# Kernel tuning notes

Hardware: AMD Instinct MI355X
Metric: run time of the kernel (lower is better)

Reference implementation:

```python
import jax, jax.numpy as jnp
import numpy as np

ROOT_2 = 1.41421
C = 256
DIV = 4
CP = C // DIV  # 64


def _spectral_normalize(w2d):
    # exact largest singular value (torch uses power iteration approx of this)
    s = jnp.linalg.norm(w2d, ord=2)
    return w2d / s


def setup_inputs() -> dict:
    key = jax.random.key(0)
    ks = jax.random.split(key, 10)
    B, H, W = 8, 64, 64
    x = jax.random.normal(ks[0], (B, C, H, W), dtype=jnp.float32)
    # 1x1 conv weights stored as [out, in]; spectral-normalized like torch's spectral_norm
    def conv_w(k, o, i):
        w = jax.random.normal(k, (o, i), dtype=jnp.float32) * (1.0 / np.sqrt(i))
        return _spectral_normalize(w)
    Wq = conv_w(ks[1], CP, C); bq = jnp.zeros((CP,), jnp.float32)
    Wk = conv_w(ks[2], CP, C); bk = jnp.zeros((CP,), jnp.float32)
    Wv = conv_w(ks[3], CP, C); bv = jnp.zeros((CP,), jnp.float32)
    Wo = conv_w(ks[4], C, CP); bo = jnp.zeros((C,), jnp.float32)
    gamma = jnp.zeros((1,), jnp.float32)
    return {"x": x, "Wq": Wq, "bq": bq, "Wk": Wk, "bk": bk,
            "Wv": Wv, "bv": bv, "Wo": Wo, "bo": bo, "gamma": gamma}


def reference(x, Wq, bq, Wk, bk, Wv, bv, Wo, bo, gamma):
    B, c, h, w = x.shape
    n = h * w
    const1 = jnp.float32(ROOT_2 / np.sqrt(C))       # Weight_Scaling(in_channels)
    const2 = jnp.float32(ROOT_2 / np.sqrt(CP))      # Weight_Scaling(in_channels//div_num)
    xs = (const1 * x).reshape(B, c, n)              # [B,C,N]
    q = jnp.einsum('oc,bcn->bon', Wq, xs) + bq[None, :, None]  # [B,C',N]
    k = jnp.einsum('oc,bcn->bon', Wk, xs) + bk[None, :, None]
    v = jnp.einsum('oc,bcn->bon', Wv, xs) + bv[None, :, None]
    # attn[b,i,j] = softmax_j(q[:,i]^T k[:,j])
    scores = jnp.einsum('bcn,bcm->bnm', q, k)       # [B,N,N]
    attn = jax.nn.softmax(scores, axis=-1)
    sa = jnp.einsum('bcm,bnm->bcn', v, attn)        # v @ attn^T
    sa = const2 * sa
    out = jnp.einsum('oc,bcn->bon', Wo, sa) + bo[None, :, None]  # [B,C,N]
    out = out.reshape(B, c, h, w)
    return gamma[0] * out + x
```

## Files before the change

kernel.cpp:

```cpp
#include <hip/hip_runtime.h>


#define Bsz 8
#define Cch 256
#define CPd 64
#define Nn  4096
#define TIL 64
#define QROWS 128
#define NSPL 4
#define MQUAR (Nn / NSPL)

typedef __attribute__((ext_vector_type(8))) short short8;
typedef __attribute__((ext_vector_type(4))) float f32x4;

static constexpr float C1 = (float)(1.41421 / 16.0);
static constexpr float C2 = (float)(1.41421 / 8.0);

__device__ inline unsigned pk_trunc(float lo, float hi) {
    return __builtin_amdgcn_perm(__float_as_uint(hi), __float_as_uint(lo), 0x07060302u);
}
__device__ inline float dpp_swap1(float v) {
    return __uint_as_float((unsigned)__builtin_amdgcn_mov_dpp(
        (int)__float_as_uint(v), 0xB1, 0xF, 0xF, true));
}
__device__ __forceinline__ void gl16(const unsigned short* g, unsigned short* s) {
    __builtin_amdgcn_global_load_lds(
        (const __attribute__((address_space(1))) void*)g,
        (__attribute__((address_space(3))) void*)s, 16, 0, 0);
}

__global__ __launch_bounds__(256) void wconv_kernel(
    const float* __restrict__ Wq, const float* __restrict__ Wk,
    const float* __restrict__ Wv, const float* __restrict__ Wo,
    unsigned short* __restrict__ Wb)
{
    const int idx = (blockIdx.x * 256 + threadIdx.x) * 4;
    const float* src = (idx < 16384) ? Wq : (idx < 32768) ? Wk : (idx < 49152) ? Wv : Wo;
    const float4 v = *(const float4*)(src + (idx & 16383));
    *(uint2*)(Wb + idx) = make_uint2(pk_trunc(v.x, v.y), pk_trunc(v.z, v.w));
}

__global__ __launch_bounds__(256) void qkv_kernel(
    const float* __restrict__ x, const unsigned short* __restrict__ Wb,
    const float* __restrict__ bq, const float* __restrict__ bk, const float* __restrict__ bv,
    unsigned short* __restrict__ qT, unsigned short* __restrict__ kT,
    unsigned short* __restrict__ vB)
{
    __shared__ __align__(16) unsigned short Wlds[CPd * 264];
    __shared__ __align__(16) float T[TIL * 68];

    const int b   = blockIdx.y;
    const int n0  = blockIdx.x * TIL;
    const int t   = threadIdx.x;
    const int g   = t >> 6;
    const int l15 = t & 15;
    const int l4  = (t & 63) >> 4;

    const float* xb = x + (size_t)b * Cch * Nn + n0 + 16 * g + l15;
    short8 xf[8];
    #pragma unroll
    for (int ks = 0; ks < 8; ++ks) {
        float xr[8];
        #pragma unroll
        for (int j = 0; j < 8; ++j)
            xr[j] = C1 * xb[(size_t)(8 * l4 + 32 * ks + j) * Nn];
        union { unsigned u[4]; short8 s; } p;
        p.u[0] = pk_trunc(xr[0], xr[1]); p.u[1] = pk_trunc(xr[2], xr[3]);
        p.u[2] = pk_trunc(xr[4], xr[5]); p.u[3] = pk_trunc(xr[6], xr[7]);
        xf[ks] = p.s;
    }

    #pragma unroll
    for (int mat = 0; mat < 3; ++mat) {
        {
            const uint4* wg = (const uint4*)(Wb + mat * 16384);
            #pragma unroll
            for (int p = 0; p < 8; ++p) {
                const int idx = p * 256 + t;
                const int o = idx >> 5, cs = idx & 31;
                *(uint4*)&Wlds[o * 264 + cs * 8] = wg[idx];
            }
        }
        __syncthreads();

        const float* bias = (mat == 0) ? bq : (mat == 1) ? bk : bv;
        f32x4 acc[4];
        #pragma unroll
        for (int st = 0; st < 4; ++st) {
            const float bb = bias[16 * st + l15];
            acc[st] = (f32x4){bb, bb, bb, bb};
        }
        #pragma unroll
        for (int st = 0; st < 4; ++st) {
            #pragma unroll
            for (int ks = 0; ks < 8; ++ks) {
                const short8 wf = *(const short8*)&Wlds[(16 * st + l15) * 264 + 8 * l4 + 32 * ks];
                acc[st] = __builtin_amdgcn_mfma_f32_16x16x32_bf16(xf[ks], wf, acc[st], 0, 0, 0);
            }
        }
        __syncthreads();

        if (mat < 2) {
            #pragma unroll
            for (int st = 0; st < 4; ++st)
                #pragma unroll
                for (int r = 0; r < 4; ++r)
                    T[(16 * g + 4 * l4 + r) * 68 + 16 * st + l15] = acc[st][r];
        } else {
            #pragma unroll
            for (int st = 0; st < 4; ++st)
                #pragma unroll
                for (int r = 0; r < 4; ++r)
                    T[(16 * st + l15) * 68 + 16 * g + 4 * l4 + r] = acc[st][r];
        }
        __syncthreads();

        const int row = t >> 2;
        const int sg  = 16 * (t & 3);
        const float4 a0 = *(const float4*)&T[row * 68 + sg + 0];
        const float4 a1 = *(const float4*)&T[row * 68 + sg + 4];
        const float4 a2 = *(const float4*)&T[row * 68 + sg + 8];
        const float4 a3 = *(const float4*)&T[row * 68 + sg + 12];
        const uint4 lo = make_uint4(pk_trunc(a0.x, a0.y), pk_trunc(a0.z, a0.w),
                                    pk_trunc(a1.x, a1.y), pk_trunc(a1.z, a1.w));
        const uint4 hi = make_uint4(pk_trunc(a2.x, a2.y), pk_trunc(a2.z, a2.w),
                                    pk_trunc(a3.x, a3.y), pk_trunc(a3.z, a3.w));
        unsigned short* dst;
        if (mat < 2) {
            dst = (mat == 0 ? qT : kT) + ((size_t)(b * Nn + n0 + row)) * CPd + sg;
        } else {
            dst = vB + ((size_t)(b * CPd + row)) * Nn + n0 + sg;
        }
        *(uint4*)dst = lo;
        *(uint4*)(dst + 8) = hi;
    }
}

__global__ __launch_bounds__(512, 6) void flash_kernel(
    const unsigned short* __restrict__ qT, const unsigned short* __restrict__ kT,
    const unsigned short* __restrict__ vB, float* __restrict__ Op, float* __restrict__ Lg)
{
    __shared__ __align__(16) unsigned short Ks0[TIL * 64];
    __shared__ __align__(16) unsigned short Ks1[TIL * 64];
    __shared__ __align__(16) unsigned short Vs0[TIL * 64];
    __shared__ __align__(16) unsigned short Vs1[TIL * 64];
    __shared__ __align__(16) unsigned Pb[QROWS * 34];

    const int b   = blockIdx.y;
    const int n0  = blockIdx.x * QROWS;
    const int s   = blockIdx.z;
    const int t   = threadIdx.x;
    const int l   = t & 63;
    const int w   = t >> 6;
    const int l15 = l & 15;
    const int l4  = l >> 4;
    const int par = l & 1;
    const unsigned sel = par ? 0x03020706u : 0x07060302u;
    const int l15h = l15 >> 1;

    const unsigned short* qp = qT + (size_t)(b * Nn + n0 + 16 * w + l15) * CPd + 8 * l4;
    const short8 qf0 = *(const short8*)qp;
    const short8 qf1 = *(const short8*)(qp + 32);

    f32x4 acco[4];
    #pragma unroll
    for (int ct = 0; ct < 4; ++ct) acco[ct] = (f32x4){0.f, 0.f, 0.f, 0.f};
    float Lp[4] = {0.f, 0.f, 0.f, 0.f};

    const int r8  = l >> 3;
    const int sch = (l & 7) ^ r8;
    const unsigned short* kPtr = kT + (size_t)b * Nn * CPd
                               + (size_t)(8 * w + r8) * CPd + 8 * sch;
    const unsigned short* vPtr = vB + (size_t)b * CPd * Nn
                               + (size_t)(8 * w + r8) * Nn + 8 * sch;
    const int ldsOff = 8 * w * 64;

    const int h7  = l15 & 7;
    const int sw0 = (l4 ^ h7) << 4;

    const int mbase = s * MQUAR;
    const int nt = MQUAR / TIL;

    auto STAGE = [&](unsigned short* KD, unsigned short* VD, int m0) {
        gl16(kPtr + (size_t)m0 * CPd, KD + ldsOff);
        gl16(vPtr + m0,               VD + ldsOff);
    };
    auto COMPUTE = [&](const unsigned short* Kb, const unsigned short* Vb) {
        const char* KsB = (const char*)Kb + (l15 << 7);
        const char* VsB = (const char*)Vb + (l15 << 7);
        f32x4 accs[4];
        __builtin_amdgcn_s_setprio(1);
        #pragma unroll
        for (int st = 0; st < 4; ++st) {
            accs[st] = (f32x4){0.f, 0.f, 0.f, 0.f};
            const short8 kf0 = *(const short8*)(KsB + (st << 11) + sw0);
            const short8 kf1 = *(const short8*)(KsB + (st << 11) + (sw0 ^ 64));
            accs[st] = __builtin_amdgcn_mfma_f32_16x16x32_bf16(qf0, kf0, accs[st], 0, 0, 0);
            accs[st] = __builtin_amdgcn_mfma_f32_16x16x32_bf16(qf1, kf1, accs[st], 0, 0, 0);
        }
        __builtin_amdgcn_s_setprio(0);
        #pragma unroll
        for (int st = 0; st < 4; ++st) {
            unsigned u[4];
            #pragma unroll
            for (int r = 0; r < 4; ++r) {
                float p = __expf(accs[st][r]);
                Lp[r] += p;
                float nb = dpp_swap1(p);
                u[r] = __builtin_amdgcn_perm(__float_as_uint(nb), __float_as_uint(p), sel);
            }
            const int rb = 16 * w + 4 * l4 + 2 * par;
            Pb[(rb + 0) * 34 + 8 * st + l15h] = u[2 * par];
            Pb[(rb + 1) * 34 + 8 * st + l15h] = u[2 * par + 1];
        }
        __builtin_amdgcn_s_setprio(1);
        #pragma unroll
        for (int ks = 0; ks < 2; ++ks) {
            const short8 pf = *(const short8*)&Pb[(16 * w + l15) * 34 + 4 * l4 + 16 * ks];
            const int swk = sw0 ^ (ks << 6);
            #pragma unroll
            for (int ct = 0; ct < 4; ++ct) {
                const short8 vf = *(const short8*)(VsB + (ct << 11) + swk);
                acco[ct] = __builtin_amdgcn_mfma_f32_16x16x32_bf16(pf, vf, acco[ct], 0, 0, 0);
            }
        }
        __builtin_amdgcn_s_setprio(0);
    };

    STAGE(Ks0, Vs0, mbase);
    __syncthreads();
    for (int ti = 0; ti < nt; ti += 2) {
        const int m0 = mbase + ti * TIL;
        STAGE(Ks1, Vs1, m0 + TIL);
        COMPUTE(Ks0, Vs0);
        __syncthreads();
        if (ti + 2 < nt) STAGE(Ks0, Vs0, m0 + 2 * TIL);
        COMPUTE(Ks1, Vs1);
        __syncthreads();
    }

    #pragma unroll
    for (int r = 0; r < 4; ++r) {
        float v = Lp[r];
        v += __shfl_xor(v, 1, 64); v += __shfl_xor(v, 2, 64);
        v += __shfl_xor(v, 4, 64); v += __shfl_xor(v, 8, 64);
        Lp[r] = v;
    }
    if (l15 == 0) {
        #pragma unroll
        for (int r = 0; r < 4; ++r)
            atomicAdd(&Lg[(size_t)b * Nn + n0 + 16 * w + 4 * l4 + r], Lp[r]);
    }
    float* ob = Op + ((size_t)(b * Nn + n0 + 16 * w)) * CPd;
    #pragma unroll
    for (int r = 0; r < 4; ++r) {
        const int nl = 4 * l4 + r;
        #pragma unroll
        for (int ct = 0; ct < 4; ++ct)
            atomicAdd(&ob[(size_t)nl * CPd + 16 * ct + l15], acco[ct][r]);
    }
}

__global__ __launch_bounds__(512) void out_kernel(
    const float* __restrict__ Op, const float* __restrict__ Lg,
    const unsigned short* __restrict__ Wob,
    const float* __restrict__ bo, const float* __restrict__ gamma,
    const float* __restrict__ x, float* __restrict__ y)
{
    __shared__ __align__(16) unsigned short Wos[Cch * 72];
    __shared__ __align__(16) unsigned short Sas[TIL * 72];
    __shared__ float bos[Cch];

    const int b   = blockIdx.y;
    const int n0  = blockIdx.x * TIL;
    const int t   = threadIdx.x;
    const int l   = t & 63;
    const int w   = t >> 6;
    const int l15 = l & 15;
    const int l4  = l >> 4;

    if (t < Cch) bos[t] = bo[t];
    {
        const uint4* wg = (const uint4*)Wob;
        #pragma unroll
        for (int p = 0; p < 4; ++p) {
            const int idx = p * 512 + t;
            const int row = idx >> 3, seg = idx & 7;
            *(uint4*)&Wos[row * 72 + seg * 8] = wg[idx];
        }
    }
    if (t < 256) {
        const int n = t >> 2, seg = t & 3;
        const float* o0 = Op + ((size_t)(b * Nn + n0 + n)) * CPd + seg * 16;
        const float sc = C2 / Lg[(size_t)b * Nn + n0 + n];
        unsigned pk[8];
        #pragma unroll
        for (int i = 0; i < 4; ++i) {
            const float4 a = ((const float4*)o0)[i];
            pk[2 * i]     = pk_trunc(a.x * sc, a.y * sc);
            pk[2 * i + 1] = pk_trunc(a.z * sc, a.w * sc);
        }
        *(uint4*)&Sas[n * 72 + seg * 16]     = make_uint4(pk[0], pk[1], pk[2], pk[3]);
        *(uint4*)&Sas[n * 72 + seg * 16 + 8] = make_uint4(pk[4], pk[5], pk[6], pk[7]);
    }
    __syncthreads();

    short8 bfr[4][2];
    #pragma unroll
    for (int ns = 0; ns < 4; ++ns) {
        bfr[ns][0] = *(const short8*)&Sas[(16 * ns + l15) * 72 + 8 * l4];
        bfr[ns][1] = *(const short8*)&Sas[(16 * ns + l15) * 72 + 8 * l4 + 32];
    }
    const float gam = gamma[0];
    const float* xb = x + (size_t)b * Cch * Nn;
    float*       yb = y + (size_t)b * Cch * Nn;

    #pragma unroll
    for (int os2 = 0; os2 < 2; ++os2) {
        const int obase = 16 * (w + 8 * os2);
        const short8 af0 = *(const short8*)&Wos[(obase + l15) * 72 + 8 * l4];
        const short8 af1 = *(const short8*)&Wos[(obase + l15) * 72 + 8 * l4 + 32];
        #pragma unroll
        for (int ns = 0; ns < 4; ++ns) {
            f32x4 acc = (f32x4){0.f, 0.f, 0.f, 0.f};
            acc = __builtin_amdgcn_mfma_f32_16x16x32_bf16(af0, bfr[ns][0], acc, 0, 0, 0);
            acc = __builtin_amdgcn_mfma_f32_16x16x32_bf16(af1, bfr[ns][1], acc, 0, 0, 0);
            #pragma unroll
            for (int r = 0; r < 4; ++r) {
                const int o = obase + 4 * l4 + r;
                const size_t idx = (size_t)o * Nn + n0 + 16 * ns + l15;
                yb[idx] = fmaf(gam, acc[r] + bos[o], xb[idx]);
            }
        }
    }
}

extern "C" void kernel_launch(void* const* d_in, const int* in_sizes, int n_in,
                              void* d_out, int out_size, void* d_ws, size_t ws_size,
                              hipStream_t stream)
{
    (void)in_sizes; (void)n_in; (void)out_size; (void)ws_size;
    const float* x     = (const float*)d_in[0];
    const float* Wq    = (const float*)d_in[1];
    const float* bq    = (const float*)d_in[2];
    const float* Wk    = (const float*)d_in[3];
    const float* bk    = (const float*)d_in[4];
    const float* Wv    = (const float*)d_in[5];
    const float* bv    = (const float*)d_in[6];
    const float* Wo    = (const float*)d_in[7];
    const float* bo    = (const float*)d_in[8];
    const float* gamma = (const float*)d_in[9];
    float* y = (float*)d_out;

    const size_t per = (size_t)Bsz * Nn * CPd;
    unsigned short* qT = (unsigned short*)d_ws;
    unsigned short* kT = qT + per;
    unsigned short* vB = kT + per;
    float* Op = (float*)(vB + per);
    float* Lg = Op + per;
    unsigned short* Wb = (unsigned short*)(Lg + (size_t)Bsz * Nn);

    hipMemsetAsync(Op, 0, (per + (size_t)Bsz * Nn) * sizeof(float), stream);

    dim3 grid(Nn / TIL, Bsz);
    dim3 gridF(Nn / QROWS, Bsz, NSPL);
    wconv_kernel<<<64, 256, 0, stream>>>(Wq, Wk, Wv, Wo, Wb);
    qkv_kernel<<<grid, 256, 0, stream>>>(x, Wb, bq, bk, bv, qT, kT, vB);
    flash_kernel<<<gridF, 512, 0, stream>>>(qT, kT, vB, Op, Lg);
    out_kernel<<<grid, 512, 0, stream>>>(Op, Lg, Wb + 3 * 16384, bo, gamma, x, y);
}
```

Measured before the change: 178.7 us.

## Single-buffer K with mid-tile barrier, XOR-swizzle P tile, fold memset into QKV kernel

The flash kernel now keeps one K buffer and double-buffers only V. The next K tile is staged after a barrier placed between the QK MFMAs and the softmax. This frees LDS so the occupancy hint can rise from 6 to 8 blocks. The padded P buffer is replaced by an XOR-swizzled 32-word row layout to avoid bank conflicts without padding. The separate hipMemsetAsync for the partial accumulators is folded into the qkv kernel as a grid-stride zero loop, which removes a launch but adds stores to that kernel and adds an extra barrier per tile.

```diff
diff --git a/kernel.cpp b/kernel.cpp
--- a/kernel.cpp
+++ b/kernel.cpp
@@ -44,7 +44,7 @@
     const float* __restrict__ x, const unsigned short* __restrict__ Wb,
     const float* __restrict__ bq, const float* __restrict__ bk, const float* __restrict__ bv,
     unsigned short* __restrict__ qT, unsigned short* __restrict__ kT,
-    unsigned short* __restrict__ vB)
+    unsigned short* __restrict__ vB, float* __restrict__ Opz)
 {
     __shared__ __align__(16) unsigned short Wlds[CPd * 264];
     __shared__ __align__(16) float T[TIL * 68];
@@ -55,6 +55,13 @@
     const int g   = t >> 6;
     const int l15 = t & 15;
     const int l4  = (t & 63) >> 4;
+
+    {
+        const int tid = (blockIdx.y * gridDim.x + blockIdx.x) * 256 + t;
+        float4* z = (float4*)Opz;
+        for (int i = tid; i < 532480; i += 131072)
+            z[i] = make_float4(0.f, 0.f, 0.f, 0.f);
+    }
 
     const float* xb = x + (size_t)b * Cch * Nn + n0 + 16 * g + l15;
     short8 xf[8];
@@ -136,15 +143,14 @@
     }
 }
 
-__global__ __launch_bounds__(512, 6) void flash_kernel(
+__global__ __launch_bounds__(512, 8) void flash_kernel(
     const unsigned short* __restrict__ qT, const unsigned short* __restrict__ kT,
     const unsigned short* __restrict__ vB, float* __restrict__ Op, float* __restrict__ Lg)
 {
-    __shared__ __align__(16) unsigned short Ks0[TIL * 64];
-    __shared__ __align__(16) unsigned short Ks1[TIL * 64];
+    __shared__ __align__(16) unsigned short Ks[TIL * 64];
     __shared__ __align__(16) unsigned short Vs0[TIL * 64];
     __shared__ __align__(16) unsigned short Vs1[TIL * 64];
-    __shared__ __align__(16) unsigned Pb[QROWS * 34];
+    __shared__ __align__(16) unsigned Pb[QROWS * 32];
 
     const int b   = blockIdx.y;
     const int n0  = blockIdx.x * QROWS;
@@ -177,17 +183,22 @@
 
     const int h7  = l15 & 7;
     const int sw0 = (l4 ^ h7) << 4;
+    const char* KsB = (const char*)Ks + (l15 << 7);
 
     const int mbase = s * MQUAR;
     const int nt = MQUAR / TIL;
 
-    auto STAGE = [&](unsigned short* KD, unsigned short* VD, int m0) {
-        gl16(kPtr + (size_t)m0 * CPd, KD + ldsOff);
-        gl16(vPtr + m0,               VD + ldsOff);
-    };
-    auto COMPUTE = [&](const unsigned short* Kb, const unsigned short* Vb) {
-        const char* KsB = (const char*)Kb + (l15 << 7);
-        const char* VsB = (const char*)Vb + (l15 << 7);
+    auto STAGE_K = [&](int m0) { gl16(kPtr + (size_t)m0 * CPd, Ks + ldsOff); };
+    auto STAGE_V = [&](unsigned short* VD, int m0) { gl16(vPtr + m0, VD + ldsOff); };
+
+    STAGE_K(mbase);
+    STAGE_V(Vs0, mbase);
+    __syncthreads();
+
+    for (int ti = 0; ti < nt; ++ti) {
+        const int m1 = mbase + (ti + 1) * TIL;
+        if (ti + 1 < nt) STAGE_V(((ti + 1) & 1) ? Vs1 : Vs0, m1);
+
         f32x4 accs[4];
         __builtin_amdgcn_s_setprio(1);
         #pragma unroll
@@ -199,6 +210,11 @@
             accs[st] = __builtin_amdgcn_mfma_f32_16x16x32_bf16(qf1, kf1, accs[st], 0, 0, 0);
         }
         __builtin_amdgcn_s_setprio(0);
+
+        asm volatile("s_waitcnt lgkmcnt(0)" ::: "memory");
+        __builtin_amdgcn_s_barrier();
+        if (ti + 1 < nt) STAGE_K(m1);
+
         #pragma unroll
         for (int st = 0; st < 4; ++st) {
             unsigned u[4];
@@ -209,14 +225,19 @@
                 float nb = dpp_swap1(p);
                 u[r] = __builtin_amdgcn_perm(__float_as_uint(nb), __float_as_uint(p), sel);
             }
-            const int rb = 16 * w + 4 * l4 + 2 * par;
-            Pb[(rb + 0) * 34 + 8 * st + l15h] = u[2 * par];
-            Pb[(rb + 1) * 34 + 8 * st + l15h] = u[2 * par + 1];
-        }
+            const int rb  = 16 * w + 4 * l4 + 2 * par;
+            const int ch  = 2 * st + (l15h >> 2);
+            const int wic = l15h & 3;
+            Pb[(rb + 0) * 32 + ((ch ^ ((rb)     & 7)) << 2) + wic] = u[2 * par];
+            Pb[(rb + 1) * 32 + ((ch ^ ((rb + 1) & 7)) << 2) + wic] = u[2 * par + 1];
+        }
+
+        const char* VsB = (const char*)((ti & 1) ? Vs1 : Vs0) + (l15 << 7);
         __builtin_amdgcn_s_setprio(1);
         #pragma unroll
         for (int ks = 0; ks < 2; ++ks) {
-            const short8 pf = *(const short8*)&Pb[(16 * w + l15) * 34 + 4 * l4 + 16 * ks];
+            const int pswz = ((l4 + 4 * ks) ^ h7) << 2;
+            const short8 pf = *(const short8*)&Pb[(16 * w + l15) * 32 + pswz];
             const int swk = sw0 ^ (ks << 6);
             #pragma unroll
             for (int ct = 0; ct < 4; ++ct) {
@@ -225,17 +246,7 @@
             }
         }
         __builtin_amdgcn_s_setprio(0);
-    };
-
-    STAGE(Ks0, Vs0, mbase);
-    __syncthreads();
-    for (int ti = 0; ti < nt; ti += 2) {
-        const int m0 = mbase + ti * TIL;
-        STAGE(Ks1, Vs1, m0 + TIL);
-        COMPUTE(Ks0, Vs0);
-        __syncthreads();
-        if (ti + 2 < nt) STAGE(Ks0, Vs0, m0 + 2 * TIL);
-        COMPUTE(Ks1, Vs1);
+
         __syncthreads();
     }
 
@@ -360,12 +371,10 @@
     float* Lg = Op + per;
     unsigned short* Wb = (unsigned short*)(Lg + (size_t)Bsz * Nn);
 
-    hipMemsetAsync(Op, 0, (per + (size_t)Bsz * Nn) * sizeof(float), stream);
-
     dim3 grid(Nn / TIL, Bsz);
     dim3 gridF(Nn / QROWS, Bsz, NSPL);
     wconv_kernel<<<64, 256, 0, stream>>>(Wq, Wk, Wv, Wo, Wb);
-    qkv_kernel<<<grid, 256, 0, stream>>>(x, Wb, bq, bk, bv, qT, kT, vB);
+    qkv_kernel<<<grid, 256, 0, stream>>>(x, Wb, bq, bk, bv, qT, kT, vB, Op);
     flash_kernel<<<gridF, 512, 0, stream>>>(qT, kT, vB, Op, Lg);
     out_kernel<<<grid, 512, 0, stream>>>(Op, Lg, Wb + 3 * 16384, bo, gamma, x, y);
 }
```

After: 205.7 us. 1.15x slower.

## Have each flash wave handle two query sub-tiles to reuse K/V fragments

Applied to the files above, without the earlier changes.

The flash kernel now runs with 256 threads, and each wave owns two 16-row query sub-tiles instead of one. Each K and V fragment read from LDS therefore feeds twice as many MFMAs, and each wave issues twice as many global-to-LDS loads per stage. The aim is to cut LDS reads per MFMA and raise arithmetic intensity per wave. The cost is higher register pressure, since the accumulators and Lp values double, and fewer waves per CU (launch bounds go from 512,6 to 256,3), which may reduce latency hiding.

```diff
diff --git a/kernel.cpp b/kernel.cpp
--- a/kernel.cpp
+++ b/kernel.cpp
@@ -136,7 +136,7 @@
     }
 }
 
-__global__ __launch_bounds__(512, 6) void flash_kernel(
+__global__ __launch_bounds__(256, 3) void flash_kernel(
     const unsigned short* __restrict__ qT, const unsigned short* __restrict__ kT,
     const unsigned short* __restrict__ vB, float* __restrict__ Op, float* __restrict__ Lg)
 {
@@ -158,14 +158,21 @@
     const unsigned sel = par ? 0x03020706u : 0x07060302u;
     const int l15h = l15 >> 1;
 
-    const unsigned short* qp = qT + (size_t)(b * Nn + n0 + 16 * w + l15) * CPd + 8 * l4;
-    const short8 qf0 = *(const short8*)qp;
-    const short8 qf1 = *(const short8*)(qp + 32);
-
-    f32x4 acco[4];
-    #pragma unroll
-    for (int ct = 0; ct < 4; ++ct) acco[ct] = (f32x4){0.f, 0.f, 0.f, 0.f};
-    float Lp[4] = {0.f, 0.f, 0.f, 0.f};
+    short8 qf[2][2];
+    #pragma unroll
+    for (int s_ = 0; s_ < 2; ++s_) {
+        const unsigned short* qp =
+            qT + (size_t)(b * Nn + n0 + 16 * (2 * w + s_) + l15) * CPd + 8 * l4;
+        qf[s_][0] = *(const short8*)qp;
+        qf[s_][1] = *(const short8*)(qp + 32);
+    }
+
+    f32x4 acco[2][4];
+    #pragma unroll
+    for (int s_ = 0; s_ < 2; ++s_)
+        #pragma unroll
+        for (int ct = 0; ct < 4; ++ct) acco[s_][ct] = (f32x4){0.f, 0.f, 0.f, 0.f};
+    float Lp[2][4] = {{0.f, 0.f, 0.f, 0.f}, {0.f, 0.f, 0.f, 0.f}};
 
     const int r8  = l >> 3;
     const int sch = (l & 7) ^ r8;
@@ -182,46 +189,58 @@
     const int nt = MQUAR / TIL;
 
     auto STAGE = [&](unsigned short* KD, unsigned short* VD, int m0) {
-        gl16(kPtr + (size_t)m0 * CPd, KD + ldsOff);
-        gl16(vPtr + m0,               VD + ldsOff);
+        gl16(kPtr + (size_t)m0 * CPd,        KD + ldsOff);
+        gl16(kPtr + (size_t)(m0 + 32) * CPd, KD + ldsOff + 32 * 64);
+        gl16(vPtr + m0,                      VD + ldsOff);
+        gl16(vPtr + (size_t)32 * Nn + m0,    VD + ldsOff + 32 * 64);
     };
     auto COMPUTE = [&](const unsigned short* Kb, const unsigned short* Vb) {
         const char* KsB = (const char*)Kb + (l15 << 7);
         const char* VsB = (const char*)Vb + (l15 << 7);
-        f32x4 accs[4];
+        f32x4 accs[2][4];
         __builtin_amdgcn_s_setprio(1);
         #pragma unroll
         for (int st = 0; st < 4; ++st) {
-            accs[st] = (f32x4){0.f, 0.f, 0.f, 0.f};
             const short8 kf0 = *(const short8*)(KsB + (st << 11) + sw0);
             const short8 kf1 = *(const short8*)(KsB + (st << 11) + (sw0 ^ 64));
-            accs[st] = __builtin_amdgcn_mfma_f32_16x16x32_bf16(qf0, kf0, accs[st], 0, 0, 0);
-            accs[st] = __builtin_amdgcn_mfma_f32_16x16x32_bf16(qf1, kf1, accs[st], 0, 0, 0);
+            #pragma unroll
+            for (int s_ = 0; s_ < 2; ++s_) {
+                accs[s_][st] = (f32x4){0.f, 0.f, 0.f, 0.f};
+                accs[s_][st] = __builtin_amdgcn_mfma_f32_16x16x32_bf16(
+                                   qf[s_][0], kf0, accs[s_][st], 0, 0, 0);
+                accs[s_][st] = __builtin_amdgcn_mfma_f32_16x16x32_bf16(
+                                   qf[s_][1], kf1, accs[s_][st], 0, 0, 0);
+            }
         }
         __builtin_amdgcn_s_setprio(0);
         #pragma unroll
-        for (int st = 0; st < 4; ++st) {
-            unsigned u[4];
-            #pragma unroll
-            for (int r = 0; r < 4; ++r) {
-                float p = __expf(accs[st][r]);
-                Lp[r] += p;
-                float nb = dpp_swap1(p);
-                u[r] = __builtin_amdgcn_perm(__float_as_uint(nb), __float_as_uint(p), sel);
-            }
-            const int rb = 16 * w + 4 * l4 + 2 * par;
-            Pb[(rb + 0) * 34 + 8 * st + l15h] = u[2 * par];
-            Pb[(rb + 1) * 34 + 8 * st + l15h] = u[2 * par + 1];
+        for (int s_ = 0; s_ < 2; ++s_) {
+            #pragma unroll
+            for (int st = 0; st < 4; ++st) {
+                unsigned u[4];
+                #pragma unroll
+                for (int r = 0; r < 4; ++r) {
+                    float p = __expf(accs[s_][st][r]);
+                    Lp[s_][r] += p;
+                    float nb = dpp_swap1(p);
+                    u[r] = __builtin_amdgcn_perm(__float_as_uint(nb), __float_as_uint(p), sel);
+                }
+                const int rb = 16 * (2 * w + s_) + 4 * l4 + 2 * par;
+                Pb[(rb + 0) * 34 + 8 * st + l15h] = u[2 * par];
+                Pb[(rb + 1) * 34 + 8 * st + l15h] = u[2 * par + 1];
+            }
         }
         __builtin_amdgcn_s_setprio(1);
         #pragma unroll
         for (int ks = 0; ks < 2; ++ks) {
-            const short8 pf = *(const short8*)&Pb[(16 * w + l15) * 34 + 4 * l4 + 16 * ks];
+            const short8 pfA = *(const short8*)&Pb[(16 * (2 * w)     + l15) * 34 + 4 * l4 + 16 * ks];
+            const short8 pfB = *(const short8*)&Pb[(16 * (2 * w + 1) + l15) * 34 + 4 * l4 + 16 * ks];
             const int swk = sw0 ^ (ks << 6);
             #pragma unroll
             for (int ct = 0; ct < 4; ++ct) {
                 const short8 vf = *(const short8*)(VsB + (ct << 11) + swk);
-                acco[ct] = __builtin_amdgcn_mfma_f32_16x16x32_bf16(pf, vf, acco[ct], 0, 0, 0);
+                acco[0][ct] = __builtin_amdgcn_mfma_f32_16x16x32_bf16(pfA, vf, acco[0][ct], 0, 0, 0);
+                acco[1][ct] = __builtin_amdgcn_mfma_f32_16x16x32_bf16(pfB, vf, acco[1][ct], 0, 0, 0);
             }
         }
         __builtin_amdgcn_s_setprio(0);
@@ -240,24 +259,28 @@
     }
 
     #pragma unroll
-    for (int r = 0; r < 4; ++r) {
-        float v = Lp[r];
-        v += __shfl_xor(v, 1, 64); v += __shfl_xor(v, 2, 64);
-        v += __shfl_xor(v, 4, 64); v += __shfl_xor(v, 8, 64);
-        Lp[r] = v;
-    }
-    if (l15 == 0) {
-        #pragma unroll
-        for (int r = 0; r < 4; ++r)
-            atomicAdd(&Lg[(size_t)b * Nn + n0 + 16 * w + 4 * l4 + r], Lp[r]);
-    }
-    float* ob = Op + ((size_t)(b * Nn + n0 + 16 * w)) * CPd;
-    #pragma unroll
-    for (int r = 0; r < 4; ++r) {
-        const int nl = 4 * l4 + r;
-        #pragma unroll
-        for (int ct = 0; ct < 4; ++ct)
-            atomicAdd(&ob[(size_t)nl * CPd + 16 * ct + l15], acco[ct][r]);
+    for (int s_ = 0; s_ < 2; ++s_) {
+        #pragma unroll
+        for (int r = 0; r < 4; ++r) {
+            float v = Lp[s_][r];
+            v += __shfl_xor(v, 1, 64); v += __shfl_xor(v, 2, 64);
+            v += __shfl_xor(v, 4, 64); v += __shfl_xor(v, 8, 64);
+            Lp[s_][r] = v;
+        }
+        if (l15 == 0) {
+            #pragma unroll
+            for (int r = 0; r < 4; ++r)
+                atomicAdd(&Lg[(size_t)b * Nn + n0 + 16 * (2 * w + s_) + 4 * l4 + r],
+                          Lp[s_][r]);
+        }
+        float* ob = Op + ((size_t)(b * Nn + n0 + 16 * (2 * w + s_))) * CPd;
+        #pragma unroll
+        for (int r = 0; r < 4; ++r) {
+            const int nl = 4 * l4 + r;
+            #pragma unroll
+            for (int ct = 0; ct < 4; ++ct)
+                atomicAdd(&ob[(size_t)nl * CPd + 16 * ct + l15], acco[s_][ct][r]);
+        }
     }
 }
 
@@ -366,6 +389,6 @@
     dim3 gridF(Nn / QROWS, Bsz, NSPL);
     wconv_kernel<<<64, 256, 0, stream>>>(Wq, Wk, Wv, Wo, Wb);
     qkv_kernel<<<grid, 256, 0, stream>>>(x, Wb, bq, bk, bv, qT, kT, vB);
-    flash_kernel<<<gridF, 512, 0, stream>>>(qT, kT, vB, Op, Lg);
+    flash_kernel<<<gridF, 256, 0, stream>>>(qT, kT, vB, Op, Lg);
     out_kernel<<<grid, 512, 0, stream>>>(Op, Lg, Wb + 3 * 16384, bo, gamma, x, y);
 }
```

New measurement: 181.2 us. About the same (+1.4%).
